# Optimization experiments

Hardware: AMD Instinct MI355X
Metric: run time of the kernel (lower is better)

The kernel has to match this reference:

```python
import jax, jax.numpy as jnp
import numpy as np

N_NODES = 20000
N_ATTRS = 5000
IN_FEATURES = 512
OUT_FEATURES = 128
ALPHA = 0.2  # LeakyReLU negative slope
NEG_INF = -9e15


def setup_inputs() -> dict:
    key = jax.random.key(0)
    k1, k2, k3, k4, k5 = jax.random.split(key, 5)
    node_embedding = jax.random.normal(k1, (N_NODES, IN_FEATURES), dtype=jnp.float32)
    attr_embedding = jax.random.normal(k2, (N_ATTRS, IN_FEATURES), dtype=jnp.float32)
    feat_mat = jax.random.randint(k3, (N_NODES, N_ATTRS), 0, 2, dtype=jnp.int32)
    # xavier_uniform with gain=1.414 (as in torch init)
    gain = 1.414
    lim_W = gain * np.sqrt(6.0 / (IN_FEATURES + OUT_FEATURES))
    W = jax.random.uniform(k4, (IN_FEATURES, OUT_FEATURES), minval=-lim_W, maxval=lim_W, dtype=jnp.float32)
    lim_a = gain * np.sqrt(6.0 / (2 * OUT_FEATURES + 1))
    a = jax.random.uniform(k5, (2 * OUT_FEATURES, 1), minval=-lim_a, maxval=lim_a, dtype=jnp.float32)
    return {"node_embedding": node_embedding, "attr_embedding": attr_embedding,
            "feat_mat": feat_mat, "W": W, "a": a}


def reference(node_embedding, attr_embedding, feat_mat, W, a):
    # Linear projections
    node_h = node_embedding @ W            # [N, F]
    attr_h = attr_embedding @ W            # [M, F]
    # Additive attention scores: e[i,j] = leakyrelu(a1.node_h[i] + a2.attr_h[j])
    wh1 = node_h @ a[:OUT_FEATURES, :]     # [N, 1]
    wh2 = attr_h @ a[OUT_FEATURES:, :]     # [M, 1]
    e = jax.nn.leaky_relu(wh1 + wh2.T, negative_slope=ALPHA)  # [N, M]
    # Mask where there is no node-attribute link, then softmax over attrs
    attention = jnp.where(feat_mat > 0, e, NEG_INF)
    attention = jax.nn.softmax(attention, axis=1)
    # (dropout is identity in eval mode)
    h_prime = attention @ attr_h           # [N, F]
    return jax.nn.elu(h_prime)             # concat=True branch
```

## Files before the change

kernel.cpp:

```cpp
#include <hip/hip_runtime.h>

#define N_NODES 20000
#define N_ATTRS 5000
#define IN_F    512
#define OUT_F   128
#define KP      5120
#define KSTEPS  160
#define NSS     80
#define WH2_PAD 5376
#define NEGBIG  -1e30f
#define LOG2E   1.4426950408889634f

typedef _Float16 f16x8 __attribute__((ext_vector_type(8)));
typedef float    f32x4 __attribute__((ext_vector_type(4)));
typedef int      i32x4 __attribute__((ext_vector_type(4)));

__device__ __forceinline__ float fast_exp2(float x) {
    return __builtin_amdgcn_exp2f(x);
}

__device__ __forceinline__ void async16(void* lds_dst, const void* gsrc) {
    __builtin_amdgcn_global_load_lds(
        (const __attribute__((address_space(1))) unsigned int*)gsrc,
        (__attribute__((address_space(3))) unsigned int*)lds_dst, 16, 0, 0);
}

__global__ __launch_bounds__(256) void prep_kernel(
    const float* __restrict__ W, const float* __restrict__ a,
    float* __restrict__ Wa1, float* __restrict__ Wa2, _Float16* __restrict__ Wp) {
    int gt = blockIdx.x * blockDim.x + threadIdx.x;
    if (gt < IN_F) {
        int k = gt;
        float s1 = 0.f, s2 = 0.f;
        for (int f = 0; f < OUT_F; ++f) {
            float w = W[k * OUT_F + f];
            s1 += w * a[f];
            s2 += w * a[OUT_F + f];
        }
        Wa1[k] = s1 * LOG2E;
        Wa2[k] = s2 * LOG2E;
    }
    for (int idx = gt; idx < IN_F * OUT_F; idx += gridDim.x * blockDim.x) {
        int j    = idx & 7;
        int lane = (idx >> 3) & 63;
        int nb   = (idx >> 9) & 7;
        int kb   = idx >> 12;
        int k = kb * 32 + (lane >> 4) * 8 + j;
        int n = nb * 16 + (lane & 15);
        Wp[idx] = (_Float16)W[k * OUT_F + n];
    }
}

__global__ __launch_bounds__(256) void wh_kernel(
    const float* __restrict__ node_emb, const float* __restrict__ attr_emb,
    const float* __restrict__ Wa1, const float* __restrict__ Wa2,
    float* __restrict__ wh1, float* __restrict__ wh2) {
    int wave = threadIdx.x >> 6, lane = threadIdx.x & 63;
    int r = blockIdx.x * 4 + wave;
    const float* src;
    const float* vec;
    float* dst;
    if (r < N_NODES) {
        src = node_emb + (size_t)r * IN_F; vec = Wa1; dst = wh1 + r;
    } else {
        int r2 = r - N_NODES;
        src = attr_emb + (size_t)r2 * IN_F; vec = Wa2; dst = wh2 + r2;
    }
    float4 ra = *reinterpret_cast<const float4*>(src + lane * 8);
    float4 rb = *reinterpret_cast<const float4*>(src + lane * 8 + 4);
    const float* vp = vec + lane * 8;
    float s = ra.x * vp[0] + ra.y * vp[1] + ra.z * vp[2] + ra.w * vp[3]
            + rb.x * vp[4] + rb.y * vp[5] + rb.z * vp[6] + rb.w * vp[7];
#pragma unroll
    for (int off = 1; off < 64; off <<= 1) s += __shfl_xor(s, off, 64);
    if (lane == 0) *dst = s;
}

__global__ __launch_bounds__(256) void max_kernel(
    float* __restrict__ wh2, float* __restrict__ maxp) {
    __shared__ float red[4];
    int t = threadIdx.x;
    float m = -1e30f;
    for (int j = t; j < N_ATTRS; j += 256) m = fmaxf(m, wh2[j]);
    for (int j = N_ATTRS + t; j < WH2_PAD; j += 256) wh2[j] = NEGBIG;
#pragma unroll
    for (int off = 1; off < 64; off <<= 1) m = fmaxf(m, __shfl_xor(m, off, 64));
    int wave = t >> 6, lane = t & 63;
    if (lane == 0) red[wave] = m;
    __syncthreads();
    if (t == 0) *maxp = fmaxf(fmaxf(red[0], red[1]), fmaxf(red[2], red[3]));
}

__global__ __launch_bounds__(256) void attr_h_kernel(
    const float* __restrict__ attr_emb, const _Float16* __restrict__ Wp,
    _Float16* __restrict__ Vp) {
    int wave = threadIdx.x >> 6, lane = threadIdx.x & 63;
    int m = lane & 15, quad = lane >> 4;
    int j0 = (blockIdx.x * 4 + wave) * 16;
    int j = j0 + m;
    bool valid = j < N_ATTRS;
    f32x4 acc[8];
#pragma unroll
    for (int nb = 0; nb < 8; ++nb)
#pragma unroll
        for (int t = 0; t < 4; ++t) acc[nb][t] = 0.f;
    const float* arow = attr_emb + (size_t)j * IN_F;
    for (int kk = 0; kk < IN_F / 32; ++kk) {
        f16x8 afrag;
        if (valid) {
            float4 ra = *reinterpret_cast<const float4*>(arow + kk * 32 + quad * 8);
            float4 rb = *reinterpret_cast<const float4*>(arow + kk * 32 + quad * 8 + 4);
            afrag[0] = (_Float16)ra.x; afrag[1] = (_Float16)ra.y;
            afrag[2] = (_Float16)ra.z; afrag[3] = (_Float16)ra.w;
            afrag[4] = (_Float16)rb.x; afrag[5] = (_Float16)rb.y;
            afrag[6] = (_Float16)rb.z; afrag[7] = (_Float16)rb.w;
        } else {
#pragma unroll
            for (int t = 0; t < 8; ++t) afrag[t] = (_Float16)0.f;
        }
        const _Float16* wbase = Wp + (size_t)(kk * 8) * 64 * 8;
#pragma unroll
        for (int nb = 0; nb < 8; ++nb) {
            f16x8 bfrag;
            __builtin_memcpy(&bfrag, wbase + (nb * 64 + lane) * 8, 16);
            acc[nb] = __builtin_amdgcn_mfma_f32_16x16x32_f16(afrag, bfrag, acc[nb], 0, 0, 0);
        }
    }
#pragma unroll
    for (int nb = 0; nb < 8; ++nb) {
#pragma unroll
        for (int reg = 0; reg < 4; ++reg) {
            int jr = j0 + quad * 4 + reg;
            int n = nb * 16 + m;
            float v = (jr < N_ATTRS) ? acc[nb][reg] : 0.f;
            size_t idx = ((size_t)((jr >> 5) * 8 + nb) * 64 +
                          (((jr >> 3) & 3) * 16 + m)) * 8 + (jr & 7);
            Vp[idx] = (_Float16)v;
        }
    }
}

__global__ __launch_bounds__(256, 3) void attn_kernel(
    const int* __restrict__ feat, const float* __restrict__ wh1,
    const float* __restrict__ wh2, const float* __restrict__ maxwh2,
    const _Float16* __restrict__ Vp, float* __restrict__ out) {
    __shared__ __align__(16) char lds[49664];
    __shared__ float rsums[32];

    int wave = threadIdx.x >> 6, lane = threadIdx.x & 63;
    int m = lane & 15, quad = lane >> 4;
    int i0 = blockIdx.x * 32;
    int rg = (wave >> 1) * 16;
    int half = wave & 1;

    float wh1i = wh1[i0 + rg + m];
    float emax = wh1i + maxwh2[0];
    float Mi = fmaxf(emax, 0.2f * emax) - 12.f;

    f32x4 acc[8];
#pragma unroll
    for (int nb = 0; nb < 8; ++nb)
#pragma unroll
        for (int t = 0; t < 4; ++t) acc[nb][t] = 0.f;
    float s = 0.f;

    char* vbuf0 = lds;
    char* fbuf0 = lds + 32768;
    char* wbuf0 = lds + 49152;

    const char* featb = (const char*)feat;
    size_t frow_off = (size_t)(i0 + rg + m) * N_ATTRS * 4;

    auto stage = [&](int ss, int b) {
        const char* vsrc = (const char*)Vp + (size_t)ss * 16384 + wave * 4096 + lane * 16;
        char* vdst = vbuf0 + b * 16384 + wave * 4096;
#pragma unroll
        for (int q = 0; q < 4; ++q) async16(vdst + q * 1024, vsrc + q * 1024);
        int kbase = (2 * ss + half) * 32;
        char* fdst = fbuf0 + b * 8192 + wave * 2048;
#pragma unroll
        for (int h = 0; h < 2; ++h) {
            int a = kbase + quad * 8 + h * 4;
            a = min(a, N_ATTRS - 4);
            async16(fdst + h * 1024, featb + frow_off + (size_t)a * 4);
        }
        if (wave == 0 && lane < 16)
            async16(wbuf0 + b * 256, (const char*)(wh2 + ss * 64) + lane * 16);
    };

    stage(0, 0);
    __syncthreads();

    for (int ss = 0; ss < NSS; ++ss) {
        int cur = ss & 1;
        if (ss + 1 < NSS) stage(ss + 1, cur ^ 1);

        char* wb = wbuf0 + cur * 256 + half * 128 + quad * 32;
        float4 wva = *reinterpret_cast<const float4*>(wb);
        float4 wvb = *reinterpret_cast<const float4*>(wb + 16);
        char* fb = fbuf0 + cur * 8192 + wave * 2048 + lane * 16;
        i32x4 fA = *reinterpret_cast<const i32x4*>(fb);
        i32x4 fB = *reinterpret_cast<const i32x4*>(fb + 1024);

        int   fi[8] = {fA.x, fA.y, fA.z, fA.w, fB.x, fB.y, fB.z, fB.w};
        float wv[8] = {wva.x, wva.y, wva.z, wva.w, wvb.x, wvb.y, wvb.z, wvb.w};
        f16x8 afrag;
#pragma unroll
        for (int t = 0; t < 8; ++t) {
            float e = wh1i + wv[t];
            float l = fmaxf(e, 0.2f * e);
            float p = fast_exp2(l - Mi);
            p = (fi[t] > 0) ? p : 0.f;
            _Float16 ph = (_Float16)p;
            s += (float)ph;
            afrag[t] = ph;
        }

        char* vb = vbuf0 + cur * 16384 + half * 8192;
#pragma unroll
        for (int nb = 0; nb < 8; ++nb) {
            f16x8 bfrag = *reinterpret_cast<const f16x8*>(vb + nb * 1024 + lane * 16);
            acc[nb] = __builtin_amdgcn_mfma_f32_16x16x32_f16(afrag, bfrag, acc[nb], 0, 0, 0);
        }

        __syncthreads();
    }

    s += __shfl_xor(s, 16, 64);
    s += __shfl_xor(s, 32, 64);

    float* accp = (float*)lds;
    if (half == 0) {
#pragma unroll
        for (int nb = 0; nb < 8; ++nb)
#pragma unroll
            for (int reg = 0; reg < 4; ++reg)
                accp[(rg + quad * 4 + reg) * 128 + nb * 16 + m] = acc[nb][reg];
        if (lane < 16) rsums[rg + lane] = s;
    }
    __syncthreads();
    if (half == 1) {
#pragma unroll
        for (int nb = 0; nb < 8; ++nb)
#pragma unroll
            for (int reg = 0; reg < 4; ++reg)
                accp[(rg + quad * 4 + reg) * 128 + nb * 16 + m] += acc[nb][reg];
        if (lane < 16) rsums[rg + lane] += s;
    }
    __syncthreads();

    for (int o = threadIdx.x; o < 32 * 128; o += 256) {
        int lr = o >> 7, n = o & 127;
        float v = accp[lr * 128 + n];
        float rs = rsums[lr];
        rs = (rs > 0.f) ? rs : 1.f;
        float h = v / rs;
        float ov = (h > 0.f) ? h : (fast_exp2(h * LOG2E) - 1.f);
        out[(size_t)(i0 + lr) * OUT_F + n] = ov;
    }
}

extern "C" void kernel_launch(void* const* d_in, const int* in_sizes, int n_in,
                              void* d_out, int out_size, void* d_ws, size_t ws_size,
                              hipStream_t stream) {
    const float* node_emb = (const float*)d_in[0];
    const float* attr_emb = (const float*)d_in[1];
    const int*   feat     = (const int*)d_in[2];
    const float* W        = (const float*)d_in[3];
    const float* a        = (const float*)d_in[4];
    float*       out      = (float*)d_out;

    char* ws = (char*)d_ws;
    float*    Wa1 = (float*)(ws + 0);
    float*    Wa2 = (float*)(ws + 4096);
    float*    wh1 = (float*)(ws + 8192);
    float*    wh2 = (float*)(ws + 90112);
    float*    mx  = (float*)(ws + 111616);
    _Float16* Wp  = (_Float16*)(ws + 131072);
    _Float16* Vp  = (_Float16*)(ws + 262144);

    prep_kernel<<<64, 256, 0, stream>>>(W, a, Wa1, Wa2, Wp);
    wh_kernel<<<6250, 256, 0, stream>>>(node_emb, attr_emb, Wa1, Wa2, wh1, wh2);
    max_kernel<<<1, 256, 0, stream>>>(wh2, mx);
    attr_h_kernel<<<80, 256, 0, stream>>>(attr_emb, Wp, Vp);
    attn_kernel<<<625, 256, 0, stream>>>(feat, wh1, wh2, mx, Vp, out);
}
```

Measured before the change: 650.4 us.

## Replace LDS double-buffered staging with register-prefetched direct global loads in attention kernel

The attention kernel drops its LDS async-copy double buffer and per-step block barriers. Each wave now handles 16 rows over the full attribute range and prefetches Vp fragments, wh2 values and an 8-step-deep ring of feat_mat rows straight into registers. Because no K-split is needed, the cross-wave LDS reduction at the end goes away and outputs are written directly from the accumulators. The cost is much higher register pressure, each wave reading Vp from global or L2 on its own with no LDS sharing, and a change to 128-thread blocks.

```diff
diff --git a/kernel.cpp b/kernel.cpp
--- a/kernel.cpp
+++ b/kernel.cpp
@@ -4,9 +4,7 @@
 #define N_ATTRS 5000
 #define IN_F    512
 #define OUT_F   128
-#define KP      5120
-#define KSTEPS  160
-#define NSS     80
+#define NK      160
 #define WH2_PAD 5376
 #define NEGBIG  -1e30f
 #define LOG2E   1.4426950408889634f
@@ -17,12 +15,6 @@
 
 __device__ __forceinline__ float fast_exp2(float x) {
     return __builtin_amdgcn_exp2f(x);
-}
-
-__device__ __forceinline__ void async16(void* lds_dst, const void* gsrc) {
-    __builtin_amdgcn_global_load_lds(
-        (const __attribute__((address_space(1))) unsigned int*)gsrc,
-        (__attribute__((address_space(3))) unsigned int*)lds_dst, 16, 0, 0);
 }
 
 __global__ __launch_bounds__(256) void prep_kernel(
@@ -140,20 +132,16 @@
     }
 }
 
-__global__ __launch_bounds__(256, 3) void attn_kernel(
+__global__ __launch_bounds__(128) void attn_kernel(
     const int* __restrict__ feat, const float* __restrict__ wh1,
     const float* __restrict__ wh2, const float* __restrict__ maxwh2,
     const _Float16* __restrict__ Vp, float* __restrict__ out) {
-    __shared__ __align__(16) char lds[49664];
-    __shared__ float rsums[32];
-
     int wave = threadIdx.x >> 6, lane = threadIdx.x & 63;
     int m = lane & 15, quad = lane >> 4;
-    int i0 = blockIdx.x * 32;
-    int rg = (wave >> 1) * 16;
-    int half = wave & 1;
-
-    float wh1i = wh1[i0 + rg + m];
+    int i0 = blockIdx.x * 32 + wave * 16;
+    int row = i0 + m;
+
+    float wh1i = wh1[row];
     float emax = wh1i + maxwh2[0];
     float Mi = fmaxf(emax, 0.2f * emax) - 12.f;
 
@@ -164,99 +152,79 @@
         for (int t = 0; t < 4; ++t) acc[nb][t] = 0.f;
     float s = 0.f;
 
-    char* vbuf0 = lds;
-    char* fbuf0 = lds + 32768;
-    char* wbuf0 = lds + 49152;
-
-    const char* featb = (const char*)feat;
-    size_t frow_off = (size_t)(i0 + rg + m) * N_ATTRS * 4;
-
-    auto stage = [&](int ss, int b) {
-        const char* vsrc = (const char*)Vp + (size_t)ss * 16384 + wave * 4096 + lane * 16;
-        char* vdst = vbuf0 + b * 16384 + wave * 4096;
-#pragma unroll
-        for (int q = 0; q < 4; ++q) async16(vdst + q * 1024, vsrc + q * 1024);
-        int kbase = (2 * ss + half) * 32;
-        char* fdst = fbuf0 + b * 8192 + wave * 2048;
-#pragma unroll
-        for (int h = 0; h < 2; ++h) {
-            int a = kbase + quad * 8 + h * 4;
-            a = min(a, N_ATTRS - 4);
-            async16(fdst + h * 1024, featb + frow_off + (size_t)a * 4);
-        }
-        if (wave == 0 && lane < 16)
-            async16(wbuf0 + b * 256, (const char*)(wh2 + ss * 64) + lane * 16);
-    };
-
-    stage(0, 0);
-    __syncthreads();
-
-    for (int ss = 0; ss < NSS; ++ss) {
-        int cur = ss & 1;
-        if (ss + 1 < NSS) stage(ss + 1, cur ^ 1);
-
-        char* wb = wbuf0 + cur * 256 + half * 128 + quad * 32;
-        float4 wva = *reinterpret_cast<const float4*>(wb);
-        float4 wvb = *reinterpret_cast<const float4*>(wb + 16);
-        char* fb = fbuf0 + cur * 8192 + wave * 2048 + lane * 16;
-        i32x4 fA = *reinterpret_cast<const i32x4*>(fb);
-        i32x4 fB = *reinterpret_cast<const i32x4*>(fb + 1024);
-
-        int   fi[8] = {fA.x, fA.y, fA.z, fA.w, fB.x, fB.y, fB.z, fB.w};
-        float wv[8] = {wva.x, wva.y, wva.z, wva.w, wvb.x, wvb.y, wvb.z, wvb.w};
-        f16x8 afrag;
-#pragma unroll
-        for (int t = 0; t < 8; ++t) {
-            float e = wh1i + wv[t];
-            float l = fmaxf(e, 0.2f * e);
-            float p = fast_exp2(l - Mi);
-            p = (fi[t] > 0) ? p : 0.f;
-            _Float16 ph = (_Float16)p;
-            s += (float)ph;
-            afrag[t] = ph;
-        }
-
-        char* vb = vbuf0 + cur * 16384 + half * 8192;
-#pragma unroll
-        for (int nb = 0; nb < 8; ++nb) {
-            f16x8 bfrag = *reinterpret_cast<const f16x8*>(vb + nb * 1024 + lane * 16);
-            acc[nb] = __builtin_amdgcn_mfma_f32_16x16x32_f16(afrag, bfrag, acc[nb], 0, 0, 0);
-        }
-
-        __syncthreads();
+    const int* fr = feat + (size_t)row * N_ATTRS;
+
+    i32x4 rA[8], rB[8];
+#pragma unroll
+    for (int u = 0; u < 8; ++u) {
+        int a = u * 32 + quad * 8;
+        rA[u] = *reinterpret_cast<const i32x4*>(fr + a);
+        rB[u] = *reinterpret_cast<const i32x4*>(fr + a + 4);
+    }
+
+    f16x8  bf[2][8];
+    float4 wva[2], wvb[2];
+    {
+        const _Float16* vb = Vp + (size_t)lane * 8;
+#pragma unroll
+        for (int nb = 0; nb < 8; ++nb)
+            bf[0][nb] = *reinterpret_cast<const f16x8*>(vb + nb * 512);
+        wva[0] = *reinterpret_cast<const float4*>(wh2 + quad * 8);
+        wvb[0] = *reinterpret_cast<const float4*>(wh2 + quad * 8 + 4);
+    }
+
+    for (int kb = 0; kb < NK; kb += 8) {
+#pragma unroll
+        for (int u = 0; u < 8; ++u) {
+            int k = kb + u;
+            int cur = u & 1, nxt = cur ^ 1;
+            int kn = (k + 1 < NK) ? (k + 1) : (NK - 1);
+            const _Float16* vbn = Vp + (size_t)kn * 4096 + lane * 8;
+#pragma unroll
+            for (int nb = 0; nb < 8; ++nb)
+                bf[nxt][nb] = *reinterpret_cast<const f16x8*>(vbn + nb * 512);
+            wva[nxt] = *reinterpret_cast<const float4*>(wh2 + kn * 32 + quad * 8);
+            wvb[nxt] = *reinterpret_cast<const float4*>(wh2 + kn * 32 + quad * 8 + 4);
+            i32x4 fa = rA[u], fb = rB[u];
+            int an = (k + 8) * 32 + quad * 8;
+            if (an > N_ATTRS - 8) an = N_ATTRS - 8;
+            rA[u] = *reinterpret_cast<const i32x4*>(fr + an);
+            rB[u] = *reinterpret_cast<const i32x4*>(fr + an + 4);
+            int   fi[8] = {fa.x, fa.y, fa.z, fa.w, fb.x, fb.y, fb.z, fb.w};
+            float wv[8] = {wva[cur].x, wva[cur].y, wva[cur].z, wva[cur].w,
+                           wvb[cur].x, wvb[cur].y, wvb[cur].z, wvb[cur].w};
+            f16x8 afrag;
+#pragma unroll
+            for (int t = 0; t < 8; ++t) {
+                float e = wh1i + wv[t];
+                float l = fmaxf(e, 0.2f * e);
+                float p = fast_exp2(l - Mi);
+                p = (fi[t] > 0) ? p : 0.f;
+                _Float16 ph = (_Float16)p;
+                s += (float)ph;
+                afrag[t] = ph;
+            }
+#pragma unroll
+            for (int nb = 0; nb < 8; ++nb)
+                acc[nb] = __builtin_amdgcn_mfma_f32_16x16x32_f16(
+                    afrag, bf[cur][nb], acc[nb], 0, 0, 0);
+        }
     }
 
     s += __shfl_xor(s, 16, 64);
     s += __shfl_xor(s, 32, 64);
 
-    float* accp = (float*)lds;
-    if (half == 0) {
-#pragma unroll
-        for (int nb = 0; nb < 8; ++nb)
-#pragma unroll
-            for (int reg = 0; reg < 4; ++reg)
-                accp[(rg + quad * 4 + reg) * 128 + nb * 16 + m] = acc[nb][reg];
-        if (lane < 16) rsums[rg + lane] = s;
-    }
-    __syncthreads();
-    if (half == 1) {
-#pragma unroll
-        for (int nb = 0; nb < 8; ++nb)
-#pragma unroll
-            for (int reg = 0; reg < 4; ++reg)
-                accp[(rg + quad * 4 + reg) * 128 + nb * 16 + m] += acc[nb][reg];
-        if (lane < 16) rsums[rg + lane] += s;
-    }
-    __syncthreads();
-
-    for (int o = threadIdx.x; o < 32 * 128; o += 256) {
-        int lr = o >> 7, n = o & 127;
-        float v = accp[lr * 128 + n];
-        float rs = rsums[lr];
+#pragma unroll
+    for (int reg = 0; reg < 4; ++reg) {
+        float rs = __shfl(s, quad * 4 + reg, 64);
         rs = (rs > 0.f) ? rs : 1.f;
-        float h = v / rs;
-        float ov = (h > 0.f) ? h : (fast_exp2(h * LOG2E) - 1.f);
-        out[(size_t)(i0 + lr) * OUT_F + n] = ov;
+        size_t ro = (size_t)(i0 + quad * 4 + reg) * OUT_F + m;
+#pragma unroll
+        for (int nb = 0; nb < 8; ++nb) {
+            float h = acc[nb][reg] / rs;
+            float ov = (h > 0.f) ? h : (fast_exp2(h * LOG2E) - 1.f);
+            out[ro + nb * 16] = ov;
+        }
     }
 }
 
@@ -283,5 +251,5 @@
     wh_kernel<<<6250, 256, 0, stream>>>(node_emb, attr_emb, Wa1, Wa2, wh1, wh2);
     max_kernel<<<1, 256, 0, stream>>>(wh2, mx);
     attr_h_kernel<<<80, 256, 0, stream>>>(attr_emb, Wp, Vp);
-    attn_kernel<<<625, 256, 0, stream>>>(feat, wh1, wh2, mx, Vp, out);
-}
+    attn_kernel<<<625, 128, 0, stream>>>(feat, wh1, wh2, mx, Vp, out);
+}
```

Result: slower. 685.3 us (+5.4%).
